# Optimization experiments

Measured on AMD Instinct MI355X. Metric: run time of the kernel, lower is better.

Reference implementation:

```python
import jax, jax.numpy as jnp
import numpy as np

EMBED = 768
HEADS = 12
HEAD_DIM = EMBED // HEADS

def setup_inputs() -> dict:
    key = jax.random.key(0)
    k1, k2, k3, k4 = jax.random.split(key, 4)
    x = jax.random.normal(k1, (8, 1024, EMBED), dtype=jnp.float32)
    # qkv Linear (no bias per qkv_bias=False); proj Linear with bias
    w_qkv = jax.random.normal(k2, (EMBED, 3 * EMBED), dtype=jnp.float32) * 0.02
    w_proj = jax.random.normal(k3, (EMBED, EMBED), dtype=jnp.float32) * 0.02
    b_proj = jax.random.normal(k4, (EMBED,), dtype=jnp.float32) * 0.02
    return {"x": x, "w_qkv": w_qkv, "w_proj": w_proj, "b_proj": b_proj}

def reference(x, w_qkv, w_proj, b_proj):
    b, n, e = x.shape
    h, d = HEADS, HEAD_DIM
    scale = d ** (-0.5)
    qkv = x @ w_qkv                                    # [b, n, 3*e]
    qkv = qkv.reshape(b, n, 3, h, d)                   # (qkv h d) split order
    q, k, v = (jnp.transpose(qkv[:, :, i], (0, 2, 1, 3)) for i in range(3))  # [b,h,n,d]
    dots = jnp.einsum('bhid,bhjd->bhij', q, k) * scale
    attn = jax.nn.softmax(dots, axis=-1)               # dropout p=0 -> identity
    out = jnp.einsum('bhij,bhjd->bhid', attn, v)       # [b,h,n,d]
    out = jnp.transpose(out, (0, 2, 1, 3)).reshape(b, n, e)
    return out @ w_proj + b_proj
```

## Files before the change

### kernel.cpp

```cpp
#include <hip/hip_runtime.h>

typedef _Float16 f16;
typedef _Float16 half8 __attribute__((ext_vector_type(8)));
typedef _Float16 half4v __attribute__((ext_vector_type(4)));
typedef __fp16 fp16x2 __attribute__((ext_vector_type(2)));
typedef float f32x4 __attribute__((ext_vector_type(4)));
typedef float f32x16 __attribute__((ext_vector_type(16)));
typedef unsigned uint4v __attribute__((ext_vector_type(4)));

#define MFMA16(a,b,c) __builtin_amdgcn_mfma_f32_16x16x32_f16((a),(b),(c),0,0,0)
#define MFMA32(a,b,c) __builtin_amdgcn_mfma_f32_32x32x16_f16((a),(b),(c),0,0,0)

__device__ __forceinline__ void gload_lds16(const f16* g, f16* l) {
    __builtin_amdgcn_global_load_lds(
        (const __attribute__((address_space(1))) unsigned int*)g,
        (__attribute__((address_space(3))) unsigned int*)l, 16, 0, 0);
}

__device__ __forceinline__ void plswap(unsigned &a, unsigned &b) {
    asm volatile("v_permlane32_swap_b32 %0, %1" : "+v"(a), "+v"(b));
}

__device__ __forceinline__ unsigned pk2(float a, float b) {
    return __builtin_bit_cast(unsigned, __builtin_amdgcn_cvt_pkrtz(a, b));
}

__device__ __forceinline__ float fexp2(float x) {
#if __has_builtin(__builtin_amdgcn_exp2f)
    return __builtin_amdgcn_exp2f(x);
#else
    return exp2f(x);
#endif
}

__device__ __forceinline__ float xswap32(float x, int hi) {
    unsigned a = __builtin_bit_cast(unsigned, x), b = a;
    asm volatile("v_permlane32_swap_b32 %0, %1" : "+v"(a), "+v"(b));
    return __builtin_bit_cast(float, hi ? a : b);
}

__global__ void cast_f32_to_f16(const float* __restrict__ in, f16* __restrict__ out, int n4) {
    int i = blockIdx.x * blockDim.x + threadIdx.x;
    if (i < n4) {
        float4 v = ((const float4*)in)[i];
        half4v h;
        h.x = (f16)v.x; h.y = (f16)v.y; h.z = (f16)v.z; h.w = (f16)v.w;
        ((half4v*)out)[i] = h;
    }
}

__global__ void transpose_cast(const float* __restrict__ in, f16* __restrict__ out, int K, int N) {
    __shared__ f16 tile[32][33];
    int n0 = blockIdx.x * 32, k0 = blockIdx.y * 32;
    int tx = threadIdx.x & 31, ty = threadIdx.x >> 5;
    for (int r = ty; r < 32; r += 8)
        tile[r][tx] = (f16)in[(size_t)(k0 + r) * N + (n0 + tx)];
    __syncthreads();
    for (int r = ty; r < 32; r += 8)
        out[(size_t)(n0 + r) * K + (k0 + tx)] = tile[tx][r];
}

template<int MODE>
__global__ __launch_bounds__(256, 3)
void gemm_bt(const f16* __restrict__ A, const f16* __restrict__ Bt,
             f16* __restrict__ qbuf, f16* __restrict__ kbuf, f16* __restrict__ vtbuf,
             float* __restrict__ out, const float* __restrict__ bias)
{
    constexpr int K = 768;
    constexpr int NX = (MODE == 0) ? 18 : 6;
    constexpr int NWG = NX * 64;
    __shared__ __align__(16) char smem[49152];
    f16* As = (f16*)smem;
    f16* Bs = (f16*)(smem + 24576);
    const int tid  = threadIdx.x;
    const int lane = tid & 63, wave = tid >> 6;
    const int wm = wave >> 1, wn = wave & 1;
    const int l15 = lane & 15, l4 = lane >> 4;

    const int bid = blockIdx.x;
    const int swz = (bid & 7) * (NWG / 8) + (bid >> 3);
    const int m0 = (swz / NX) * 128, n0 = (swz % NX) * 128;

    const int srow  = lane >> 2;
    const int sslot = lane & 3;

    f32x4 acc[4][4] = {};

    #define GSTAGE(buf, kt) do {                                                     \
        _Pragma("unroll")                                                            \
        for (int i = 0; i < 2; ++i) {                                                \
            int rbase = i * 64 + wave * 16;                                          \
            int row = rbase + srow;                                                  \
            gload_lds16(A  + (size_t)(m0 + row) * K + (kt) + sslot * 8, &As[(buf) * 4096 + rbase * 32]); \
            gload_lds16(Bt + (size_t)(n0 + row) * K + (kt) + sslot * 8, &Bs[(buf) * 4096 + rbase * 32]); \
        }                                                                            \
    } while (0)

    GSTAGE(0, 0);
    GSTAGE(1, 32);

    int cur = 0;
    for (int t = 0; t < 24; ++t) {
        if (t < 23) asm volatile("s_waitcnt vmcnt(4)" ::: "memory");
        else        asm volatile("s_waitcnt vmcnt(0)" ::: "memory");
        __builtin_amdgcn_s_barrier();
        if (t < 22) {
            int nb = cur + 2; if (nb >= 3) nb -= 3;
            GSTAGE(nb, (t + 2) * 32);
        }
        half8 af[4], bf[4];
        #pragma unroll
        for (int mi = 0; mi < 4; mi++) af[mi] = *(const half8*)&As[cur*4096 + (wm*64 + mi*16 + l15) * 32 + l4*8];
        #pragma unroll
        for (int ni = 0; ni < 4; ni++) bf[ni] = *(const half8*)&Bs[cur*4096 + (wn*64 + ni*16 + l15) * 32 + l4*8];
        #pragma unroll
        for (int mi = 0; mi < 4; mi++)
            #pragma unroll
            for (int ni = 0; ni < 4; ni++)
                acc[mi][ni] = MFMA16(af[mi], bf[ni], acc[mi][ni]);
        if (++cur >= 3) cur = 0;
    }
    #undef GSTAGE

    if (MODE == 0) {
        __syncthreads();
        f16* sC = (f16*)smem;
        const int t3 = n0 / 768;
        const int bb = m0 >> 10;
        const int mo = m0 & 1023;
        const int h0 = (n0 - t3 * 768) >> 6;

        if (t3 < 2) {
            #pragma unroll
            for (int mi = 0; mi < 4; mi++)
                #pragma unroll
                for (int ni = 0; ni < 4; ni++)
                    #pragma unroll
                    for (int r = 0; r < 4; r++) {
                        int row = wm*64 + mi*16 + l4*4 + r;
                        int col = wn*64 + ni*16 + l15;
                        sC[row * 136 + col] = (f16)acc[mi][ni][r];
                    }
            __syncthreads();
            f16* outb = (t3 == 0) ? qbuf : kbuf;
            #pragma unroll
            for (int hc = 0; hc < 2; hc++) {
                f16* base = outb + ((size_t)(bb * 12 + h0 + hc) * 1024 + mo) * 64;
                #pragma unroll
                for (int i = 0; i < 4; i++) {
                    int row = wave * 32 + i * 8 + (lane >> 3);
                    int cc  = (lane & 7) * 8;
                    half8 v = *(const half8*)&sC[row * 136 + hc * 64 + cc];
                    *(half8*)(base + row * 64 + cc) = v;
                }
            }
        } else {
            #pragma unroll
            for (int mi = 0; mi < 4; mi++)
                #pragma unroll
                for (int ni = 0; ni < 4; ni++) {
                    int row0 = wm*64 + mi*16 + l4*4;
                    int col  = wn*64 + ni*16 + l15;
                    half4v pk;
                    #pragma unroll
                    for (int r = 0; r < 4; r++) pk[r] = (f16)acc[mi][ni][r];
                    *(half4v*)&sC[col * 136 + row0] = pk;
                }
            __syncthreads();
            #pragma unroll
            for (int i = 0; i < 8; i++) {
                int col = wave * 32 + i * 4 + (lane >> 4);
                int rc  = (lane & 15) * 8;
                half8 v = *(const half8*)&sC[col * 136 + rc];
                int head = h0 + (col >> 6), dd = col & 63;
                *(half8*)(vtbuf + ((size_t)(bb * 12 + head) * 64 + dd) * 1024 + mo + rc) = v;
            }
        }
    } else {
        #pragma unroll
        for (int mi = 0; mi < 4; mi++)
            #pragma unroll
            for (int ni = 0; ni < 4; ni++)
                #pragma unroll
                for (int r = 0; r < 4; r++) {
                    int gm = m0 + wm*64 + mi*16 + l4*4 + r;
                    int gn = n0 + wn*64 + ni*16 + l15;
                    out[(size_t)gm * 768 + gn] = acc[mi][ni][r] + bias[gn];
                }
    }
}

__global__ __launch_bounds__(256, 3)
void attn_kernel(const f16* __restrict__ qbuf, const f16* __restrict__ kbuf,
                 const f16* __restrict__ vtbuf, f16* __restrict__ obuf)
{
    __shared__ __align__(16) f16 Ks[3][4096];
    __shared__ __align__(16) f16 Vs[3][4096];
    const int tid = threadIdx.x;
    const int lane = tid & 63, wave = tid >> 6;
    const int bh = blockIdx.x;
    const int b = bh / 12, h = bh % 12;
    const int q0 = blockIdx.y * 128 + wave * 32;
    const int l31 = lane & 31, hi = lane >> 5;
    const int sw0 = (l31 & 7) << 4;

    const f16* Q  = qbuf  + (size_t)bh * 65536;
    const f16* Kp = kbuf  + (size_t)bh * 65536;
    const f16* Vt = vtbuf + (size_t)bh * 65536;

    const f16 slh = (f16)(0.125f * 1.44269504089f);
    half8 aq[4];
    #pragma unroll
    for (int c = 0; c < 4; c++) {
        aq[c] = *(const half8*)&Q[(size_t)(q0 + l31) * 64 + c * 16 + hi * 8];
        #pragma unroll
        for (int j = 0; j < 8; j++) aq[c][j] *= slh;
    }

    const int srow8 = lane >> 3;
    const int c16   = (lane & 7) ^ srow8;

    f32x16 o0 = {}, o1 = {};
    float lrq = 0.f, mrq = 0.f, stale = 0.f;

    #define STAGE(buf, kv) do {                                                     \
        _Pragma("unroll")                                                           \
        for (int i = 0; i < 2; ++i) {                                               \
            int rbase = wave * 16 + i * 8;                                          \
            int rl = rbase + srow8;                                                 \
            gload_lds16(Kp + (size_t)((kv) + rl) * 64 + c16 * 8, &Ks[buf][rbase * 64]); \
            gload_lds16(Vt + (size_t)rl * 1024 + (kv) + c16 * 8, &Vs[buf][rbase * 64]); \
        }                                                                           \
    } while (0)

    #define QKISSUE(dst0, dst1, kb, minit) do {                                     \
        _Pragma("unroll")                                                           \
        for (int j = 0; j < 16; j++) { dst0[j] = (minit); dst1[j] = (minit); }      \
        __builtin_amdgcn_s_setprio(1);                                              \
        _Pragma("unroll")                                                           \
        for (int c = 0; c < 4; c++) {                                               \
            int koff = (c * 32 + hi * 16) ^ sw0;                                    \
            half8 k0 = *(const half8*)((kb) + l31 * 128 + koff);                    \
            half8 k1 = *(const half8*)((kb) + (32 + l31) * 128 + koff);             \
            dst0 = MFMA32(k0, aq[c], dst0);                                         \
            dst1 = MFMA32(k1, aq[c], dst1);                                         \
        }                                                                           \
        __builtin_amdgcn_s_setprio(0);                                              \
    } while (0)

    STAGE(0, 0);
    STAGE(1, 64);
    __syncthreads();

    f32x16 st0, st1;
    QKISSUE(st0, st1, (const char*)&Ks[0][0], 0.f);

    int bcur = 0;
    for (int t = 0; t < 16; ++t) {
        int bn1 = bcur + 1; if (bn1 >= 3) bn1 -= 3;
        int bn2 = bcur + 2; if (bn2 >= 3) bn2 -= 3;

        if (t < 14) STAGE(bn2, (t + 2) * 64);

        f32x16 sN0, sN1;
        if (t < 15) QKISSUE(sN0, sN1, (const char*)&Ks[bn1][0], -mrq);

        if (__any(stale != 0.f)) {
            #pragma unroll
            for (int j = 0; j < 16; j++) { st0[j] -= stale; st1[j] -= stale; }
        }
        stale = 0.f;

        float m16;
        {
            float p0 = fmaxf(fmaxf(st0[0],  st0[1]),  fmaxf(st0[2],  st0[3]));
            float p1 = fmaxf(fmaxf(st0[4],  st0[5]),  fmaxf(st0[6],  st0[7]));
            float p2 = fmaxf(fmaxf(st0[8],  st0[9]),  fmaxf(st0[10], st0[11]));
            float p3 = fmaxf(fmaxf(st0[12], st0[13]), fmaxf(st0[14], st0[15]));
            float r0 = fmaxf(fmaxf(st1[0],  st1[1]),  fmaxf(st1[2],  st1[3]));
            float r1 = fmaxf(fmaxf(st1[4],  st1[5]),  fmaxf(st1[6],  st1[7]));
            float r2 = fmaxf(fmaxf(st1[8],  st1[9]),  fmaxf(st1[10], st1[11]));
            float r3 = fmaxf(fmaxf(st1[12], st1[13]), fmaxf(st1[14], st1[15]));
            m16 = fmaxf(fmaxf(fmaxf(p0, p1), fmaxf(p2, p3)),
                        fmaxf(fmaxf(r0, r1), fmaxf(r2, r3)));
        }
        m16 = fmaxf(m16, xswap32(m16, hi));

        if (!__all(m16 <= 11.0f)) {
            float d = fmaxf(m16, 0.f);
            float alpha = fexp2(-d);
            mrq += d;
            stale = d;
            #pragma unroll
            for (int j = 0; j < 16; j++) { st0[j] -= d; st1[j] -= d; }
            lrq *= alpha;
            #pragma unroll
            for (int reg = 0; reg < 16; reg++) {
                float a = __shfl(alpha, (reg & 3) + 8 * (reg >> 2) + 4 * hi);
                o0[reg] *= a; o1[reg] *= a;
            }
        }

        float rs = 0.f;
        half8 pa[4];
        #pragma unroll
        for (int tile = 0; tile < 2; tile++) {
            const f32x16& sv = tile ? st1 : st0;
            #pragma unroll
            for (int half16 = 0; half16 < 2; half16++) {
                int rb = half16 * 8;
                unsigned A1, B1, A2, B2;
                {
                    float e0 = fexp2(sv[rb+0]), e1 = fexp2(sv[rb+1]);
                    float e4 = fexp2(sv[rb+4]), e5 = fexp2(sv[rb+5]);
                    rs += (e0 + e1) + (e4 + e5);
                    A1 = pk2(e0, e1); B1 = pk2(e4, e5);
                    plswap(A1, B1);
                }
                {
                    float e2 = fexp2(sv[rb+2]), e3 = fexp2(sv[rb+3]);
                    float e6 = fexp2(sv[rb+6]), e7 = fexp2(sv[rb+7]);
                    rs += (e2 + e3) + (e6 + e7);
                    A2 = pk2(e2, e3); B2 = pk2(e6, e7);
                    plswap(A2, B2);
                }
                uint4v w = {A1, A2, B1, B2};
                pa[tile * 2 + half16] = __builtin_bit_cast(half8, w);
            }
        }
        rs += xswap32(rs, hi);
        lrq += rs;

        {
            const char* Vb = (const char*)&Vs[bcur][0];
            __builtin_amdgcn_s_setprio(1);
            #pragma unroll
            for (int kc = 0; kc < 4; kc++) {
                int koff = (kc * 32 + hi * 16) ^ sw0;
                half8 v0 = *(const half8*)(Vb + l31 * 128 + koff);
                half8 v1 = *(const half8*)(Vb + (32 + l31) * 128 + koff);
                o0 = MFMA32(pa[kc], v0, o0);
                o1 = MFMA32(pa[kc], v1, o1);
            }
            __builtin_amdgcn_s_setprio(0);
        }

        if (t < 15) {
            asm volatile("s_waitcnt vmcnt(0)" ::: "memory");
            __builtin_amdgcn_s_barrier();
            st0 = sN0; st1 = sN1;
        }
        bcur = bn1;
    }
    #undef QKISSUE
    #undef STAGE

    float rq = 1.0f / lrq;
    f16* Op = obuf + (size_t)b * 1024 * 768 + h * 64;
    #pragma unroll
    for (int reg = 0; reg < 16; reg++) {
        int qrow = (reg & 3) + 8 * (reg >> 2) + 4 * hi;
        float inv = __shfl(rq, qrow);
        size_t base = (size_t)(q0 + qrow) * 768;
        Op[base + l31]      = (f16)(o0[reg] * inv);
        Op[base + 32 + l31] = (f16)(o1[reg] * inv);
    }
}

extern "C" void kernel_launch(void* const* d_in, const int* in_sizes, int n_in,
                              void* d_out, int out_size, void* d_ws, size_t ws_size,
                              hipStream_t stream) {
    const float* x      = (const float*)d_in[0];
    const float* w_qkv  = (const float*)d_in[1];
    const float* w_proj = (const float*)d_in[2];
    const float* b_proj = (const float*)d_in[3];
    float* out = (float*)d_out;
    char* ws = (char*)d_ws;

    f16* x_h      = (f16*)(ws + 0);
    f16* w_qkv_t  = (f16*)(ws + 12582912);
    f16* w_proj_t = (f16*)(ws + 16121856);
    f16* qb       = (f16*)(ws + 17301504);
    f16* kb       = (f16*)(ws + 29884416);
    f16* vtb      = (f16*)(ws + 42467328);
    f16* ob       = (f16*)(ws + 55050240);

    cast_f32_to_f16<<<dim3(6144), dim3(256), 0, stream>>>(x, x_h, 6291456 / 4);
    transpose_cast<<<dim3(2304 / 32, 768 / 32), dim3(256), 0, stream>>>(w_qkv, w_qkv_t, 768, 2304);
    transpose_cast<<<dim3(768 / 32, 768 / 32), dim3(256), 0, stream>>>(w_proj, w_proj_t, 768, 768);
    gemm_bt<0><<<dim3(18 * 64), dim3(256), 0, stream>>>(
        x_h, w_qkv_t, qb, kb, vtb, nullptr, nullptr);
    attn_kernel<<<dim3(96, 8), dim3(256), 0, stream>>>(qb, kb, vtb, ob);
    gemm_bt<1><<<dim3(6 * 64), dim3(256), 0, stream>>>(
        ob, w_proj_t, nullptr, nullptr, nullptr, out, b_proj);
}
```

Baseline: 121.1 us.

## Split QKV GEMM into dedicated 128x256-tile kernel using 32x32 MFMA

Splits the templated GEMM into a dedicated QKV kernel and a projection kernel. The QKV kernel now uses 128x256 tiles with 32x32x16 MFMA instructions, swizzled LDS chunk placement to reduce bank conflicts, and a larger 72KB shared buffer at occupancy 2. The aim is more operand reuse per loaded tile and fewer LDS reads per MFMA for the largest GEMM. The cost is fewer workgroups (576 on a 256-CU part, about 2.25 waves) and lower occupancy, which could hurt latency hiding and tail balance.

```diff
diff --git a/kernel.cpp b/kernel.cpp
--- a/kernel.cpp
+++ b/kernel.cpp
@@ -60,14 +60,148 @@
         out[(size_t)(n0 + r) * K + (k0 + tx)] = tile[tx][r];
 }
 
-template<int MODE>
-__global__ __launch_bounds__(256, 3)
-void gemm_bt(const f16* __restrict__ A, const f16* __restrict__ Bt,
-             f16* __restrict__ qbuf, f16* __restrict__ kbuf, f16* __restrict__ vtbuf,
-             float* __restrict__ out, const float* __restrict__ bias)
+__global__ __launch_bounds__(256, 2)
+void gemm_qkv(const f16* __restrict__ A, const f16* __restrict__ Bt,
+              f16* __restrict__ qbuf, f16* __restrict__ kbuf, f16* __restrict__ vtbuf)
 {
     constexpr int K = 768;
-    constexpr int NX = (MODE == 0) ? 18 : 6;
+    constexpr int NX = 9;
+    constexpr int NWG = 64 * NX;
+    __shared__ __align__(16) char smem[73728];
+    f16* As = (f16*)smem;
+    f16* Bs = (f16*)(smem + 24576);
+    const int tid  = threadIdx.x;
+    const int lane = tid & 63, wave = tid >> 6;
+    const int wm = wave >> 1, wn = wave & 1;
+    const int l31 = lane & 31, hi = lane >> 5;
+
+    const int bid = blockIdx.x;
+    const int swz = (bid & 7) * (NWG / 8) + (bid >> 3);
+    const int m0 = (swz / NX) * 128;
+    const int ntile = swz % NX;
+    const int n0 = ntile * 256;
+
+    const int srow = lane >> 2;
+    const int schunk = ((lane & 3) - (srow & 3)) & 3;
+
+    f32x16 acc[2][4] = {};
+
+    #define GSTAGE(buf, kt) do {                                                         \
+        _Pragma("unroll")                                                                \
+        for (int i = 0; i < 2; ++i) {                                                    \
+            int rb = i * 64 + wave * 16;                                                 \
+            gload_lds16(A + (size_t)(m0 + rb + srow) * K + (kt) + schunk * 8,            \
+                        &As[(buf) * 4096 + rb * 32]);                                    \
+        }                                                                                \
+        _Pragma("unroll")                                                                \
+        for (int j = 0; j < 4; ++j) {                                                    \
+            int rb = j * 64 + wave * 16;                                                 \
+            gload_lds16(Bt + (size_t)(n0 + rb + srow) * K + (kt) + schunk * 8,           \
+                        &Bs[(buf) * 8192 + rb * 32]);                                    \
+        }                                                                                \
+    } while (0)
+
+    GSTAGE(0, 0);
+    GSTAGE(1, 32);
+
+    int cur = 0;
+    for (int t = 0; t < 24; ++t) {
+        if (t < 23) asm volatile("s_waitcnt vmcnt(6)" ::: "memory");
+        else        asm volatile("s_waitcnt vmcnt(0)" ::: "memory");
+        __builtin_amdgcn_s_barrier();
+        if (t < 22) {
+            int nb = cur + 2; if (nb >= 3) nb -= 3;
+            GSTAGE(nb, (t + 2) * 32);
+        }
+        #pragma unroll
+        for (int ks = 0; ks < 2; ks++) {
+            half8 af[2], bf[4];
+            #pragma unroll
+            for (int mt = 0; mt < 2; mt++) {
+                int row = wm * 64 + mt * 32 + l31;
+                int slot = (ks * 2 + hi + row) & 3;
+                af[mt] = *(const half8*)&As[cur * 4096 + row * 32 + slot * 8];
+            }
+            #pragma unroll
+            for (int nt = 0; nt < 4; nt++) {
+                int row = wn * 128 + nt * 32 + l31;
+                int slot = (ks * 2 + hi + row) & 3;
+                bf[nt] = *(const half8*)&Bs[cur * 8192 + row * 32 + slot * 8];
+            }
+            #pragma unroll
+            for (int mt = 0; mt < 2; mt++)
+                #pragma unroll
+                for (int nt = 0; nt < 4; nt++)
+                    acc[mt][nt] = MFMA32(af[mt], bf[nt], acc[mt][nt]);
+        }
+        if (++cur >= 3) cur = 0;
+    }
+    #undef GSTAGE
+
+    __syncthreads();
+    const int t3 = ntile / 3;
+    const int bb = m0 >> 10;
+    const int mo = m0 & 1023;
+    const int h0 = (ntile % 3) * 4;
+
+    if (t3 < 2) {
+        f16* sC = (f16*)smem;
+        #pragma unroll
+        for (int mt = 0; mt < 2; mt++)
+            #pragma unroll
+            for (int nt = 0; nt < 4; nt++)
+                #pragma unroll
+                for (int reg = 0; reg < 16; reg++) {
+                    int row = wm * 64 + mt * 32 + (reg & 3) + 8 * (reg >> 2) + 4 * hi;
+                    int col = wn * 128 + nt * 32 + l31;
+                    sC[row * 264 + col] = (f16)acc[mt][nt][reg];
+                }
+        __syncthreads();
+        f16* outb = (t3 == 0) ? qbuf : kbuf;
+        #pragma unroll
+        for (int hc = 0; hc < 4; hc++) {
+            f16* base = outb + ((size_t)(bb * 12 + h0 + hc) * 1024 + mo) * 64;
+            #pragma unroll
+            for (int i = 0; i < 4; i++) {
+                int row = i * 32 + (tid >> 3);
+                int c   = (tid & 7) * 8;
+                half8 v = *(const half8*)&sC[row * 264 + hc * 64 + c];
+                *(half8*)(base + row * 64 + c) = v;
+            }
+        }
+    } else {
+        f16* sC = (f16*)smem;
+        #pragma unroll
+        for (int mt = 0; mt < 2; mt++)
+            #pragma unroll
+            for (int nt = 0; nt < 4; nt++) {
+                int col = wn * 128 + nt * 32 + l31;
+                #pragma unroll
+                for (int q4 = 0; q4 < 4; q4++) {
+                    half4v pk;
+                    #pragma unroll
+                    for (int r = 0; r < 4; r++) pk[r] = (f16)acc[mt][nt][q4 * 4 + r];
+                    *(half4v*)&sC[col * 136 + wm * 64 + mt * 32 + q4 * 8 + hi * 4] = pk;
+                }
+            }
+        __syncthreads();
+        #pragma unroll
+        for (int i = 0; i < 16; i++) {
+            int col = i * 16 + (tid >> 4);
+            int rc  = (tid & 15) * 8;
+            half8 v = *(const half8*)&sC[col * 136 + rc];
+            int head = h0 + (col >> 6), dd = col & 63;
+            *(half8*)(vtbuf + ((size_t)(bb * 12 + head) * 64 + dd) * 1024 + mo + rc) = v;
+        }
+    }
+}
+
+__global__ __launch_bounds__(256, 3)
+void gemm_proj(const f16* __restrict__ A, const f16* __restrict__ Bt,
+               float* __restrict__ out, const float* __restrict__ bias)
+{
+    constexpr int K = 768;
+    constexpr int NX = 6;
     constexpr int NWG = NX * 64;
     __shared__ __align__(16) char smem[49152];
     f16* As = (f16*)smem;
@@ -122,72 +256,16 @@
     }
     #undef GSTAGE
 
-    if (MODE == 0) {
-        __syncthreads();
-        f16* sC = (f16*)smem;
-        const int t3 = n0 / 768;
-        const int bb = m0 >> 10;
-        const int mo = m0 & 1023;
-        const int h0 = (n0 - t3 * 768) >> 6;
-
-        if (t3 < 2) {
-            #pragma unroll
-            for (int mi = 0; mi < 4; mi++)
-                #pragma unroll
-                for (int ni = 0; ni < 4; ni++)
-                    #pragma unroll
-                    for (int r = 0; r < 4; r++) {
-                        int row = wm*64 + mi*16 + l4*4 + r;
-                        int col = wn*64 + ni*16 + l15;
-                        sC[row * 136 + col] = (f16)acc[mi][ni][r];
-                    }
-            __syncthreads();
-            f16* outb = (t3 == 0) ? qbuf : kbuf;
-            #pragma unroll
-            for (int hc = 0; hc < 2; hc++) {
-                f16* base = outb + ((size_t)(bb * 12 + h0 + hc) * 1024 + mo) * 64;
-                #pragma unroll
-                for (int i = 0; i < 4; i++) {
-                    int row = wave * 32 + i * 8 + (lane >> 3);
-                    int cc  = (lane & 7) * 8;
-                    half8 v = *(const half8*)&sC[row * 136 + hc * 64 + cc];
-                    *(half8*)(base + row * 64 + cc) = v;
-                }
-            }
-        } else {
-            #pragma unroll
-            for (int mi = 0; mi < 4; mi++)
-                #pragma unroll
-                for (int ni = 0; ni < 4; ni++) {
-                    int row0 = wm*64 + mi*16 + l4*4;
-                    int col  = wn*64 + ni*16 + l15;
-                    half4v pk;
-                    #pragma unroll
-                    for (int r = 0; r < 4; r++) pk[r] = (f16)acc[mi][ni][r];
-                    *(half4v*)&sC[col * 136 + row0] = pk;
-                }
-            __syncthreads();
-            #pragma unroll
-            for (int i = 0; i < 8; i++) {
-                int col = wave * 32 + i * 4 + (lane >> 4);
-                int rc  = (lane & 15) * 8;
-                half8 v = *(const half8*)&sC[col * 136 + rc];
-                int head = h0 + (col >> 6), dd = col & 63;
-                *(half8*)(vtbuf + ((size_t)(bb * 12 + head) * 64 + dd) * 1024 + mo + rc) = v;
-            }
-        }
-    } else {
-        #pragma unroll
-        for (int mi = 0; mi < 4; mi++)
-            #pragma unroll
-            for (int ni = 0; ni < 4; ni++)
-                #pragma unroll
-                for (int r = 0; r < 4; r++) {
-                    int gm = m0 + wm*64 + mi*16 + l4*4 + r;
-                    int gn = n0 + wn*64 + ni*16 + l15;
-                    out[(size_t)gm * 768 + gn] = acc[mi][ni][r] + bias[gn];
-                }
-    }
+    #pragma unroll
+    for (int mi = 0; mi < 4; mi++)
+        #pragma unroll
+        for (int ni = 0; ni < 4; ni++)
+            #pragma unroll
+            for (int r = 0; r < 4; r++) {
+                int gm = m0 + wm*64 + mi*16 + l4*4 + r;
+                int gn = n0 + wn*64 + ni*16 + l15;
+                out[(size_t)gm * 768 + gn] = acc[mi][ni][r] + bias[gn];
+            }
 }
 
 __global__ __launch_bounds__(256, 3)
@@ -388,9 +466,7 @@
     cast_f32_to_f16<<<dim3(6144), dim3(256), 0, stream>>>(x, x_h, 6291456 / 4);
     transpose_cast<<<dim3(2304 / 32, 768 / 32), dim3(256), 0, stream>>>(w_qkv, w_qkv_t, 768, 2304);
     transpose_cast<<<dim3(768 / 32, 768 / 32), dim3(256), 0, stream>>>(w_proj, w_proj_t, 768, 768);
-    gemm_bt<0><<<dim3(18 * 64), dim3(256), 0, stream>>>(
-        x_h, w_qkv_t, qb, kb, vtb, nullptr, nullptr);
+    gemm_qkv<<<dim3(64 * 9), dim3(256), 0, stream>>>(x_h, w_qkv_t, qb, kb, vtb);
     attn_kernel<<<dim3(96, 8), dim3(256), 0, stream>>>(qb, kb, vtb, ob);
-    gemm_bt<1><<<dim3(6 * 64), dim3(256), 0, stream>>>(
-        ob, w_proj_t, nullptr, nullptr, nullptr, out, b_proj);
-}
+    gemm_proj<<<dim3(64 * 6), dim3(256), 0, stream>>>(ob, w_proj_t, out, b_proj);
+}
```

Result: slower. 127.3 us (+5.2%).
